# Kernel optimization log

Hardware: AMD Instinct MI355X
Metric: run time of the kernel (lower is better)

## Reference

```python
import jax, jax.numpy as jnp
import numpy as np

B, N, E_PER_G = 32, 2048, 16384
NF, NHID, NCLS = 128, 128, 10
RATIO = 0.5
NT = B * N
E = B * E_PER_G
K1 = int(np.ceil(RATIO * N))        # 1024 nodes kept per graph after pool1
K2 = int(np.ceil(RATIO * K1))       # 512
K3 = int(np.ceil(RATIO * K2))       # 256


def setup_inputs() -> dict:
    key = jax.random.key(0)
    ks = jax.random.split(key, 16)
    x = jax.random.normal(ks[0], (NT, NF), dtype=jnp.float32)
    off = (jnp.arange(B, dtype=jnp.int32) * N)[:, None]
    src = (jax.random.randint(ks[1], (B, E_PER_G), 0, N, dtype=jnp.int32) + off).reshape(-1)
    dst = (jax.random.randint(ks[2], (B, E_PER_G), 0, N, dtype=jnp.int32) + off).reshape(-1)
    edge_index = jnp.stack([src, dst])
    batch = jnp.repeat(jnp.arange(B, dtype=jnp.int32), N)
    def lin(k, i, o):
        return jax.random.normal(k, (i, o), jnp.float32) / np.float32(np.sqrt(i))
    return {
        'x': x, 'edge_index': edge_index, 'batch': batch,
        'W1': lin(ks[3], NF, NHID), 'b1': jnp.zeros((NHID,), jnp.float32),
        'Wp1': lin(ks[4], NHID, 1), 'bp1': jnp.zeros((1,), jnp.float32),
        'W2': lin(ks[5], NHID, NHID), 'b2': jnp.zeros((NHID,), jnp.float32),
        'Wp2': lin(ks[6], NHID, 1), 'bp2': jnp.zeros((1,), jnp.float32),
        'W3': lin(ks[7], NHID, NHID), 'b3': jnp.zeros((NHID,), jnp.float32),
        'Wp3': lin(ks[8], NHID, 1), 'bp3': jnp.zeros((1,), jnp.float32),
        'lin1_W': lin(ks[9], 2 * NHID, NHID), 'lin1_b': jnp.zeros((NHID,), jnp.float32),
        'lin2_W': lin(ks[10], NHID, NHID // 2), 'lin2_b': jnp.zeros((NHID // 2,), jnp.float32),
        'lin3_W': lin(ks[11], NHID // 2, NCLS), 'lin3_b': jnp.zeros((NCLS,), jnp.float32),
    }


def gcn(x, src, dst, emask, nmask, W, b):
    # PyG GCNConv: add self-loops, symmetric normalization D^-1/2 (A+I) D^-1/2 @ (x W) + b.
    # Removed nodes/edges carry weight 0 via masks (equivalent to filter_adj re-indexing).
    h = x @ W
    deg = jnp.zeros((NT,), h.dtype).at[dst].add(emask) + nmask
    dinv = jnp.where(deg > 0, 1.0, 0.0) * jax.lax.rsqrt(jnp.where(deg > 0, deg, 1.0))
    coef = dinv[src] * dinv[dst] * emask               # [E]
    out = jnp.zeros_like(h).at[dst].add(coef[:, None] * h[src])
    out = out + ((dinv * dinv) * nmask)[:, None] * h   # self-loop term, norm = 1/deg
    return out + b


def sagpool(x, src, dst, emask, nmask, Wp, bp, k):
    # score = GCNConv(nhid,1); keep top-k per graph; x <- x[perm] * tanh(score[perm])
    score = gcn(x, src, dst, emask, nmask, Wp, bp)[:, 0]          # [NT]
    s = jnp.where(nmask > 0, score, -jnp.inf).reshape(B, N)
    _, idx = jax.lax.top_k(s, k)                                   # [B, k]
    keep = jnp.zeros((B, N), x.dtype).at[jnp.arange(B)[:, None], idx].set(1.0).reshape(-1)
    x_new = x * jnp.tanh(score)[:, None] * keep[:, None]
    emask_new = emask * keep[src] * keep[dst]                      # filter_adj
    return x_new, emask_new, keep


def readout(x, nmask, count):
    # [global_max_pool, global_mean_pool] over active nodes of each graph
    xb = x.reshape(B, N, -1)
    m = nmask.reshape(B, N, 1)
    mx = jnp.max(jnp.where(m > 0, xb, -jnp.inf), axis=1)
    mn = jnp.sum(xb * m, axis=1) / count
    return jnp.concatenate([mx, mn], axis=-1)


def reference(x, edge_index, batch, W1, b1, Wp1, bp1, W2, b2, Wp2, bp2,
              W3, b3, Wp3, bp3, lin1_W, lin1_b, lin2_W, lin2_b, lin3_W, lin3_b):
    src, dst = edge_index[0], edge_index[1]
    emask = jnp.ones((E,), x.dtype)
    nmask = jnp.ones((NT,), x.dtype)

    h = jax.nn.relu(gcn(x, src, dst, emask, nmask, W1, b1))
    h, emask, nmask = sagpool(h, src, dst, emask, nmask, Wp1, bp1, K1)
    x1 = readout(h, nmask, jnp.asarray(K1, x.dtype))

    h = jax.nn.relu(gcn(h, src, dst, emask, nmask, W2, b2))
    h, emask, nmask = sagpool(h, src, dst, emask, nmask, Wp2, bp2, K2)
    x2 = readout(h, nmask, jnp.asarray(K2, x.dtype))

    h = jax.nn.relu(gcn(h, src, dst, emask, nmask, W3, b3))
    h, emask, nmask = sagpool(h, src, dst, emask, nmask, Wp3, bp3, K3)
    x3 = readout(h, nmask, jnp.asarray(K3, x.dtype))

    g = x1 + x2 + x3
    g = jax.nn.relu(g @ lin1_W + lin1_b)   # dropout = identity in eval
    g = jax.nn.relu(g @ lin2_W + lin2_b)
    return jax.nn.log_softmax(g @ lin3_W + lin3_b, axis=-1)
```

## Files before the change

### kernel.cpp

```cpp
#include <hip/hip_runtime.h>
#include <math.h>


namespace {

constexpr int B_  = 32;
constexpr int N_  = 2048;
constexpr int NT  = B_ * N_;
constexpr int EPG = 16384;
constexpr int E_  = B_ * EPG;
constexpr int NCLS = 10;
constexpr int AST = 132;

__device__ __forceinline__ int relabel(int bid, int bpgsh) {
  int x = bid & 7, slot = bid >> 3;
  int g = x + 8 * (slot >> bpgsh);
  return (g << bpgsh) + (slot & ((1 << bpgsh) - 1));
}

__device__ void csr_build(const int* __restrict__ src, const int* __restrict__ dst,
                          int* __restrict__ off, int* __restrict__ srcp,
                          float* __restrict__ dinv, float* __restrict__ ds,
                          float* __restrict__ sws, int* hist) {
  const int g = blockIdx.x;
  const int t = threadIdx.x;
  const int base_n = g * N_;
  const int base_e = g * EPG;
  int* wsum8 = hist + 2048;
#pragma unroll
  for (int i = 0; i < 4; ++i) hist[t + 512 * i] = 0;
  __syncthreads();
  for (int i = 0; i < EPG / 512; i += 8) {
    int dd[8];
#pragma unroll
    for (int j = 0; j < 8; ++j) dd[j] = dst[base_e + t + 512 * (i + j)];
#pragma unroll
    for (int j = 0; j < 8; ++j) atomicAdd(&hist[dd[j] - base_n], 1);
  }
  __syncthreads();
  int a[4], ssum = 0;
#pragma unroll
  for (int i = 0; i < 4; ++i) { a[i] = hist[4 * t + i]; ssum += a[i]; }
  {
    int lane = t & 63, w = t >> 6;
    int v = ssum;
#pragma unroll
    for (int o = 1; o < 64; o <<= 1) {
      int nv = __shfl_up(v, o);
      if (lane >= o) v += nv;
    }
    if (lane == 63) wsum8[w] = v;
    __syncthreads();
    if (t == 0) {
      int accv = 0;
      for (int i = 0; i < 8; ++i) { int tmp = wsum8[i]; wsum8[i] = accv; accv += tmp; }
    }
    __syncthreads();
    int run = wsum8[w] + v - ssum;
#pragma unroll
    for (int i = 0; i < 4; ++i) {
      int n = 4 * t + i;
      off[base_n + n] = base_e + run;
      hist[n] = run;
      float d0 = 1.f + (float)a[i];
      float di0 = 1.f / sqrtf(d0);
      dinv[base_n + n] = di0;
      ds[base_n + n] = di0;
      sws[base_n + n] = di0 * di0;
      run += a[i];
    }
    if (g == B_ - 1 && t == 0) off[NT] = E_;
  }
  __syncthreads();
  for (int i = 0; i < EPG / 512; i += 8) {
    int dd[8], ss[8];
#pragma unroll
    for (int j = 0; j < 8; ++j) {
      int e = base_e + t + 512 * (i + j);
      dd[j] = dst[e];
      ss[j] = src[e];
    }
#pragma unroll
    for (int j = 0; j < 8; ++j) {
      int slot = atomicAdd(&hist[dd[j] - base_n], 1);
      srcp[base_e + slot] = ss[j];
    }
  }
}

__device__ void norm_body(const int* __restrict__ off,
                          const int* __restrict__ srcp,
                          const float* __restrict__ kpmask,
                          const float* __restrict__ scale,
                          float* __restrict__ dinv,
                          float* __restrict__ ds,
                          float* __restrict__ sws,
                          const int* __restrict__ nkept,
                          int nkshift, int nbpgsh, int nb) {
  int q = relabel(nb, nbpgsh) * 64 + ((int)threadIdx.x >> 3);
  int g = q >> nkshift;
  int node = nkept[g * N_ + (q - (g << nkshift))];
  const int lane = threadIdx.x & 7;
  int s = off[node], en = off[node + 1];
  float d = (lane == 0) ? 1.f : 0.f;
  for (int j = s + lane; j < en; j += 8) d += kpmask[srcp[j]];
#pragma unroll
  for (int o = 4; o >= 1; o >>= 1) d += __shfl_down(d, o, 8);
  if (lane == 0) {
    float di = 1.f / sqrtf(d);
    float sc = scale[node];
    dinv[node] = di;
    ds[node] = di * sc;
    sws[node] = di * di * sc;
  }
}

__global__ __launch_bounds__(512) void k_matmul(const float* __restrict__ A,
                                                const float* __restrict__ W,
                                                float* __restrict__ C,
                                                const int* __restrict__ kept,
                                                int kshift, int bpgsh, int mmBlocks,
                                                const float* __restrict__ scaleArr,
                                                float* __restrict__ pmx,
                                                float* __restrict__ psm,
                                                const int* __restrict__ src,
                                                const int* __restrict__ dst,
                                                int* __restrict__ off,
                                                int* __restrict__ srcp,
                                                float* __restrict__ dinvW,
                                                float* __restrict__ dsW,
                                                float* __restrict__ swsW,
                                                int csrBlocks,
                                                const float* __restrict__ kpmask,
                                                const int* __restrict__ nkept,
                                                int nkshift, int nbpgsh) {
  __shared__ float Ast[2][32 * AST];
  __shared__ float Ws[2][32 * 128];
  __shared__ int rowid[128];
  __shared__ float rsc[128];
  if ((int)blockIdx.x < csrBlocks) {
    csr_build(src, dst, off, srcp, dinvW, dsW, swsW, (int*)&Ast[0][0]);
    return;
  }
  if ((int)blockIdx.x >= csrBlocks + mmBlocks) {
    norm_body(off, srcp, kpmask, scaleArr, dinvW, dsW, swsW, nkept,
              nkshift, nbpgsh, (int)blockIdx.x - csrBlocks - mmBlocks);
    return;
  }
  const int tid = threadIdx.x;
  const int tile = relabel((int)blockIdx.x - csrBlocks, bpgsh);
  if (kept) {
    if (tid < 128) {
      int q = tile * 128 + tid;
      int g = q >> kshift;
      int row = kept[g * N_ + (q - (g << kshift))];
      rowid[tid] = row;
      rsc[tid] = scaleArr[row];
    }
    __syncthreads();
  }
  const int rowq = tid >> 4;
  const int colq = tid & 15;
  float4 va[2], vw[2];
#pragma unroll
  for (int i = 0; i < 2; ++i) {
    int idx = tid + 512 * i;
    int row = idx >> 3, f4 = idx & 7;
    int grw = kept ? rowid[row] : tile * 128 + row;
    va[i] = *(const float4*)&A[(size_t)grw * 128 + 4 * f4];
  }
#pragma unroll
  for (int i = 0; i < 2; ++i) {
    int idx = tid + 512 * i;
    int kk = idx >> 5, cf = idx & 31;
    vw[i] = *(const float4*)&W[(size_t)kk * 128 + 4 * cf];
  }
#pragma unroll
  for (int i = 0; i < 2; ++i) {
    int idx = tid + 512 * i;
    int row = idx >> 3, f4 = idx & 7;
    Ast[0][(4 * f4 + 0) * AST + row] = va[i].x;
    Ast[0][(4 * f4 + 1) * AST + row] = va[i].y;
    Ast[0][(4 * f4 + 2) * AST + row] = va[i].z;
    Ast[0][(4 * f4 + 3) * AST + row] = va[i].w;
  }
#pragma unroll
  for (int i = 0; i < 2; ++i) {
    int idx = tid + 512 * i;
    int kk = idx >> 5, cf = idx & 31;
    *(float4*)&Ws[0][kk * 128 + 4 * cf] = vw[i];
  }
  __syncthreads();
  float acc[4][8] = {};
  for (int c = 0; c < 4; ++c) {
    int cur = c & 1;
    if (c < 3) {
      int k0n = 32 * (c + 1);
#pragma unroll
      for (int i = 0; i < 2; ++i) {
        int idx = tid + 512 * i;
        int row = idx >> 3, f4 = idx & 7;
        int grw = kept ? rowid[row] : tile * 128 + row;
        va[i] = *(const float4*)&A[(size_t)grw * 128 + k0n + 4 * f4];
      }
#pragma unroll
      for (int i = 0; i < 2; ++i) {
        int idx = tid + 512 * i;
        int kk = idx >> 5, cf = idx & 31;
        vw[i] = *(const float4*)&W[(size_t)(k0n + kk) * 128 + 4 * cf];
      }
    }
#pragma unroll 2
    for (int kk = 0; kk < 32; ++kk) {
      float4 a0 = *(const float4*)&Ast[cur][kk * AST + 4 * rowq];
      float4 w0 = *(const float4*)&Ws[cur][kk * 128 + 4 * colq];
      float4 w1 = *(const float4*)&Ws[cur][kk * 128 + 64 + 4 * colq];
      float a[4] = {a0.x, a0.y, a0.z, a0.w};
      float w[8] = {w0.x, w0.y, w0.z, w0.w, w1.x, w1.y, w1.z, w1.w};
#pragma unroll
      for (int r = 0; r < 4; ++r)
#pragma unroll
        for (int cc = 0; cc < 8; ++cc) acc[r][cc] += a[r] * w[cc];
    }
    if (kept) {
      int kkf = tid >> 4;
      int r0 = (tid & 15) * 8;
      float mxv = -INFINITY, smv = 0.f;
#pragma unroll
      for (int rr = 0; rr < 8; rr += 4) {
        float4 av = *(const float4*)&Ast[cur][kkf * AST + r0 + rr];
        float4 s4 = *(const float4*)&rsc[r0 + rr];
        float v0 = av.x * s4.x, v1 = av.y * s4.y;
        float v2 = av.z * s4.z, v3 = av.w * s4.w;
        mxv = fmaxf(fmaxf(fmaxf(mxv, v0), fmaxf(v1, v2)), v3);
        smv += v0 + v1 + v2 + v3;
      }
#pragma unroll
      for (int o = 8; o >= 1; o >>= 1) {
        mxv = fmaxf(mxv, __shfl_down(mxv, o, 16));
        smv += __shfl_down(smv, o, 16);
      }
      if ((tid & 15) == 0) {
        pmx[(size_t)tile * 128 + 32 * c + kkf] = mxv;
        psm[(size_t)tile * 128 + 32 * c + kkf] = smv;
      }
    }
    if (c < 3) {
      int nxt = cur ^ 1;
#pragma unroll
      for (int i = 0; i < 2; ++i) {
        int idx = tid + 512 * i;
        int row = idx >> 3, f4 = idx & 7;
        Ast[nxt][(4 * f4 + 0) * AST + row] = va[i].x;
        Ast[nxt][(4 * f4 + 1) * AST + row] = va[i].y;
        Ast[nxt][(4 * f4 + 2) * AST + row] = va[i].z;
        Ast[nxt][(4 * f4 + 3) * AST + row] = va[i].w;
      }
#pragma unroll
      for (int i = 0; i < 2; ++i) {
        int idx = tid + 512 * i;
        int kk = idx >> 5, cf = idx & 31;
        *(float4*)&Ws[nxt][kk * 128 + 4 * cf] = vw[i];
      }
      __syncthreads();
    }
  }
#pragma unroll
  for (int r = 0; r < 4; ++r) {
    int grw = kept ? rowid[4 * rowq + r] : tile * 128 + 4 * rowq + r;
    float* Crow = &C[(size_t)grw * 128];
    *(float4*)&Crow[4 * colq] = make_float4(acc[r][0], acc[r][1], acc[r][2], acc[r][3]);
    *(float4*)&Crow[64 + 4 * colq] = make_float4(acc[r][4], acc[r][5], acc[r][6], acc[r][7]);
  }
}

__global__ __launch_bounds__(256) void k_agg(const float4* __restrict__ t4,
                                             const int* __restrict__ off,
                                             const int* __restrict__ srcp,
                                             const float* __restrict__ dinv,
                                             const float* __restrict__ ds,
                                             const float* __restrict__ sws,
                                             const float* __restrict__ bias,
                                             const float* __restrict__ Wp,
                                             float4* __restrict__ h4,
                                             float* __restrict__ t1,
                                             const int* __restrict__ kept,
                                             int kshift, int bpgsh) {
  int q = relabel(blockIdx.x, bpgsh) * 8 + (threadIdx.x >> 5);
  int node;
  if (kept) {
    int g = q >> kshift;
    node = kept[g * N_ + (q - (g << kshift))];
  } else {
    node = q;
  }
  const int lane = threadIdx.x & 31;
  const float dvi = dinv[node];
  float sw = sws[node];
  float4 self = t4[(size_t)node * 32 + lane];
  float4 acc = make_float4(sw * self.x, sw * self.y, sw * self.z, sw * self.w);
  int s = off[node], en = off[node + 1];
  int j = s;
  for (; j + 8 <= en; j += 8) {
    int sv[8];
    float cv[8];
#pragma unroll
    for (int i = 0; i < 8; ++i) sv[i] = srcp[j + i];
#pragma unroll
    for (int i = 0; i < 8; ++i) cv[i] = ds[sv[i]] * dvi;
#pragma unroll
    for (int i = 0; i < 8; ++i) {
      if (cv[i] != 0.f) {
        float4 r = t4[(size_t)sv[i] * 32 + lane];
        acc.x += cv[i] * r.x; acc.y += cv[i] * r.y;
        acc.z += cv[i] * r.z; acc.w += cv[i] * r.w;
      }
    }
  }
  for (; j < en; ++j) {
    int s0 = srcp[j];
    float c0 = ds[s0] * dvi;
    if (c0 != 0.f) {
      float4 r0 = t4[(size_t)s0 * 32 + lane];
      acc.x += c0 * r0.x; acc.y += c0 * r0.y; acc.z += c0 * r0.z; acc.w += c0 * r0.w;
    }
  }
  float4 b4 = ((const float4*)bias)[lane];
  acc.x = fmaxf(acc.x + b4.x, 0.f);
  acc.y = fmaxf(acc.y + b4.y, 0.f);
  acc.z = fmaxf(acc.z + b4.z, 0.f);
  acc.w = fmaxf(acc.w + b4.w, 0.f);
  h4[(size_t)node * 32 + lane] = acc;
  float4 wp = ((const float4*)Wp)[lane];
  float part = acc.x * wp.x + acc.y * wp.y + acc.z * wp.z + acc.w * wp.w;
#pragma unroll
  for (int o = 16; o > 0; o >>= 1) part += __shfl_down(part, o, 32);
  if (lane == 0) t1[node] = part;
}

__global__ __launch_bounds__(256) void k_score(const float* __restrict__ t1,
                                               const int* __restrict__ off,
                                               const int* __restrict__ srcp,
                                               const float* __restrict__ dinv,
                                               const float* __restrict__ bp,
                                               float* __restrict__ raw,
                                               const int* __restrict__ kept,
                                               int kshift, int bpgsh) {
  int q = relabel(blockIdx.x, bpgsh) * 32 + (threadIdx.x >> 3);
  int node;
  if (kept) {
    int g = q >> kshift;
    node = kept[g * N_ + (q - (g << kshift))];
  } else {
    node = q;
  }
  const int lane = threadIdx.x & 7;
  int s = off[node], en = off[node + 1];
  float a = 0.f;
  for (int j = s + lane; j < en; j += 8) {
    int sl = srcp[j];
    a += dinv[sl] * t1[sl];
  }
#pragma unroll
  for (int o = 4; o >= 1; o >>= 1) a += __shfl_down(a, o, 8);
  if (lane == 0) {
    float di = dinv[node];
    raw[node] = di * di * t1[node] + di * a + bp[0];
  }
}

__global__ __launch_bounds__(1024) void k_pool(const float* __restrict__ raw,
                                               float* __restrict__ dinv,
                                               float* __restrict__ ds,
                                               float* __restrict__ sws,
                                               float* __restrict__ scale,
                                               float* __restrict__ kpmask,
                                               int* __restrict__ kept,
                                               const float4* __restrict__ h4,
                                               float invk, int k,
                                               const int* __restrict__ inKept, int klen,
                                               const float* __restrict__ pmxA,
                                               const float* __restrict__ psmA,
                                               const float* __restrict__ pmxB,
                                               const float* __restrict__ psmB,
                                               const float* __restrict__ hW1,
                                               const float* __restrict__ hb1,
                                               const float* __restrict__ hW2,
                                               const float* __restrict__ hb2,
                                               const float* __restrict__ hW3,
                                               const float* __restrict__ hb3,
                                               float* __restrict__ out) {
  __shared__ float st1[2048];
  __shared__ float skp[2048];
  __shared__ int skept[1024];
  __shared__ unsigned rephist[4096];
  __shared__ unsigned ebits[64];
  __shared__ int wsum[16];
  __shared__ unsigned bc_digit, bc_prev;
  __shared__ float gr[256], o1[128], o2[64], o3[NCLS];
  const int g = (blockIdx.x & 7) + 8 * (blockIdx.x >> 3);
  const int t = threadIdx.x;
  const int base = g * N_;
  st1[t] = 0.f;
  st1[t + 1024] = 0.f;
  skp[t] = 0.f;
  skp[t + 1024] = 0.f;
  if (t < 64) ebits[t] = 0u;
  __syncthreads();
  int nodeq[2] = {-1, -1};
  float rawv[2] = {0.f, 0.f};
  unsigned key[2] = {0xFFFFFFFFu, 0xFFFFFFFFu};
#pragma unroll
  for (int q = 0; q < 2; ++q) {
    int i = t + q * 1024;
    if (i >= klen) continue;
    int n = inKept ? (inKept[base + i] - base) : i;
    nodeq[q] = n;
    float r = raw[base + n];
    rawv[q] = r;
    unsigned u = __float_as_uint(r);
    u = (u & 0x80000000u) ? ~u : (u | 0x80000000u);
    u = ~u;
    key[q] = u;
  }
  unsigned prefix = 0u, rem = (unsigned)k;
  const int SH0 = 21, SH1 = 10, SH2 = 0;
  for (int p = 0; p < 3; ++p) {
    const int shift = (p == 0) ? SH0 : (p == 1 ? SH1 : SH2);
    const int nb = (p == 2) ? 1024 : 2048;
    const unsigned mask = (p == 0) ? 0u
                        : (p == 1 ? (0xFFFFFFFFu << SH0) : (0xFFFFFFFFu << SH1));
    rephist[t] = 0u;
    rephist[t + 1024] = 0u;
    __syncthreads();
#pragma unroll
    for (int q = 0; q < 2; ++q)
      if (nodeq[q] >= 0 && (key[q] & mask) == prefix)
        atomicAdd(&rephist[(key[q] >> shift) & (unsigned)(nb - 1)], 1u);
    __syncthreads();
    unsigned b0, b1;
    if (nb == 2048) { b0 = rephist[2 * t]; b1 = rephist[2 * t + 1]; }
    else           { b0 = rephist[t];     b1 = 0u; }
    unsigned ps = b0 + b1;
    {
      int lane = t & 63, w = t >> 6;
      unsigned v = ps;
#pragma unroll
      for (int o = 1; o < 64; o <<= 1) {
        unsigned nv = __shfl_up(v, o);
        if (lane >= o) v += nv;
      }
      if (lane == 63) wsum[w] = (int)v;
      __syncthreads();
      if (t == 0) {
        int accv = 0;
        for (int i = 0; i < 16; ++i) { int tmp = wsum[i]; wsum[i] = accv; accv += tmp; }
      }
      __syncthreads();
      unsigned exc = (unsigned)wsum[w] + v - ps;
      if (exc < rem && exc + b0 >= rem) {
        bc_digit = (unsigned)((nb == 2048) ? 2 * t : t);
        bc_prev = exc;
      }
      if (nb == 2048 && exc + b0 < rem && exc + b0 + b1 >= rem) {
        bc_digit = (unsigned)(2 * t + 1);
        bc_prev = exc + b0;
      }
    }
    __syncthreads();
    prefix |= bc_digit << shift;
    rem -= bc_prev;
  }
  const unsigned Tkey = prefix;
  const int need = (int)rem;
#pragma unroll
  for (int q = 0; q < 2; ++q) {
    int n = nodeq[q];
    if (n >= 0 && key[q] == Tkey) atomicOr(&ebits[n >> 5], 1u << (n & 31));
  }
  __syncthreads();
#pragma unroll
  for (int q = 0; q < 2; ++q) {
    int n = nodeq[q];
    if (n < 0) continue;
    float kp;
    if (key[q] < Tkey) {
      kp = 1.f;
    } else if (key[q] == Tkey) {
      int w = n >> 5;
      int rank = __popc(ebits[w] & ((1u << (n & 31)) - 1u));
      for (int u = 0; u < w; ++u) rank += __popc(ebits[u]);
      kp = (rank < need) ? 1.f : 0.f;
    } else {
      kp = 0.f;
    }
    skp[n] = kp;
    float sc = kp * tanhf(rawv[q]);
    st1[n] = sc;
    scale[base + n] = sc;
    kpmask[base + n] = kp;
    if (kp == 0.f) {
      dinv[base + n] = 0.f;
      ds[base + n] = 0.f;
      sws[base + n] = 0.f;
    }
  }
  __syncthreads();
  {
    int lane = t & 63, w = t >> 6;
    int a0 = (int)skp[2 * t], a1 = (int)skp[2 * t + 1];
    int ps = a0 + a1;
    int v = ps;
#pragma unroll
    for (int o = 1; o < 64; o <<= 1) {
      int nv = __shfl_up(v, o);
      if (lane >= o) v += nv;
    }
    if (lane == 63) wsum[w] = v;
    __syncthreads();
    if (t == 0) {
      int accv = 0;
      for (int i = 0; i < 16; ++i) { int tmp = wsum[i]; wsum[i] = accv; accv += tmp; }
    }
    __syncthreads();
    int excl = wsum[w] + v - ps;
    if (a0) { kept[base + excl] = base + 2 * t; skept[excl] = base + 2 * t; }
    if (a1) { kept[base + excl + a0] = base + 2 * t + 1; skept[excl + a0] = base + 2 * t + 1; }
  }
  if (!out) return;
  __syncthreads();
  const int lane = t & 31, ng = t >> 5;
  float4 mx = make_float4(-INFINITY, -INFINITY, -INFINITY, -INFINITY);
  float4 sm = make_float4(0.f, 0.f, 0.f, 0.f);
  for (int i = ng; i < k; i += 32) {
    int node = skept[i];
    float sc = st1[node - base];
    float4 v = h4[(size_t)node * 32 + lane];
    v.x *= sc; v.y *= sc; v.z *= sc; v.w *= sc;
    mx.x = fmaxf(mx.x, v.x); mx.y = fmaxf(mx.y, v.y);
    mx.z = fmaxf(mx.z, v.z); mx.w = fmaxf(mx.w, v.w);
    sm.x += v.x; sm.y += v.y; sm.z += v.z; sm.w += v.w;
  }
  float4* red = (float4*)rephist;
  for (int d = 16; d >= 1; d >>= 1) {
    if (ng >= d && ng < 2 * d) {
      red[(ng - d) * 32 + lane] = mx;
      red[512 + (ng - d) * 32 + lane] = sm;
    }
    __syncthreads();
    if (ng < d) {
      float4 omx = red[ng * 32 + lane];
      float4 osm = red[512 + ng * 32 + lane];
      mx.x = fmaxf(mx.x, omx.x); mx.y = fmaxf(mx.y, omx.y);
      mx.z = fmaxf(mx.z, omx.z); mx.w = fmaxf(mx.w, omx.w);
      sm.x += osm.x; sm.y += osm.y; sm.z += osm.z; sm.w += osm.w;
    }
    __syncthreads();
  }
  if (ng == 0) {
    gr[4 * lane + 0] = mx.x;
    gr[4 * lane + 1] = mx.y;
    gr[4 * lane + 2] = mx.z;
    gr[4 * lane + 3] = mx.w;
    gr[128 + 4 * lane + 0] = sm.x * invk;
    gr[128 + 4 * lane + 1] = sm.y * invk;
    gr[128 + 4 * lane + 2] = sm.z * invk;
    gr[128 + 4 * lane + 3] = sm.w * invk;
  }
  __syncthreads();
  if (t < 128) {
    float mxA = -INFINITY, smA = 0.f;
#pragma unroll
    for (int p = 0; p < 8; ++p) {
      mxA = fmaxf(mxA, pmxA[(size_t)(g * 8 + p) * 128 + t]);
      smA += psmA[(size_t)(g * 8 + p) * 128 + t];
    }
    float mxB = -INFINITY, smB = 0.f;
#pragma unroll
    for (int p = 0; p < 4; ++p) {
      mxB = fmaxf(mxB, pmxB[(size_t)(g * 4 + p) * 128 + t]);
      smB += psmB[(size_t)(g * 4 + p) * 128 + t];
    }
    gr[t] += mxA + mxB;
    gr[t + 128] += smA * (1.f / 1024.f) + smB * (1.f / 512.f);
  }
  __syncthreads();
  if (t < 128) {
    float a = hb1[t];
    for (int kk = 0; kk < 256; ++kk) a += gr[kk] * hW1[kk * 128 + t];
    o1[t] = fmaxf(a, 0.f);
  }
  __syncthreads();
  if (t < 64) {
    float a2 = hb2[t];
    for (int kk = 0; kk < 128; ++kk) a2 += o1[kk] * hW2[kk * 64 + t];
    o2[t] = fmaxf(a2, 0.f);
  }
  __syncthreads();
  if (t < NCLS) {
    float a3 = hb3[t];
    for (int kk = 0; kk < 64; ++kk) a3 += o2[kk] * hW3[kk * NCLS + t];
    o3[t] = a3;
  }
  __syncthreads();
  if (t == 0) {
    float m = -INFINITY;
    for (int c = 0; c < NCLS; ++c) m = fmaxf(m, o3[c]);
    float sum = 0.f;
    for (int c = 0; c < NCLS; ++c) sum += expf(o3[c] - m);
    float lse = logf(sum);
    for (int c = 0; c < NCLS; ++c) out[g * NCLS + c] = o3[c] - m - lse;
  }
}

}

extern "C" void kernel_launch(void* const* d_in, const int* in_sizes, int n_in,
                              void* d_out, int out_size, void* d_ws, size_t ws_size,
                              hipStream_t stream) {
  const float* x = (const float*)d_in[0];
  const int* ei = (const int*)d_in[1];
  const int* src = ei;
  const int* dst = ei + E_;
  const float* Wl[3]  = {(const float*)d_in[3], (const float*)d_in[7], (const float*)d_in[11]};
  const float* bl[3]  = {(const float*)d_in[4], (const float*)d_in[8], (const float*)d_in[12]};
  const float* Wpl[3] = {(const float*)d_in[5], (const float*)d_in[9], (const float*)d_in[13]};
  const float* bpl[3] = {(const float*)d_in[6], (const float*)d_in[10], (const float*)d_in[14]};
  const float* l1W = (const float*)d_in[15];
  const float* l1b = (const float*)d_in[16];
  const float* l2W = (const float*)d_in[17];
  const float* l2b = (const float*)d_in[18];
  const float* l3W = (const float*)d_in[19];
  const float* l3b = (const float*)d_in[20];

  char* p = (char*)d_ws;
  auto alloc = [&](size_t bytes) -> void* {
    void* r = (void*)p;
    p += (bytes + 255) & ~size_t(255);
    return r;
  };
  float* h      = (float*)alloc((size_t)NT * 128 * 4);
  float* t      = (float*)alloc((size_t)NT * 128 * 4);
  float* dinv   = (float*)alloc(NT * 4);
  float* ds     = (float*)alloc(NT * 4);
  float* sws    = (float*)alloc(NT * 4);
  float* scale  = (float*)alloc(NT * 4);
  float* t1     = (float*)alloc(NT * 4);
  float* raw    = (float*)alloc(NT * 4);
  float* kpmask = (float*)alloc(NT * 4);
  int*   srcp   = (int*)alloc(E_ * 4);
  int*   off    = (int*)alloc((NT + 1) * 4);
  int*   kept0  = (int*)alloc(NT * 4);
  int*   kept1  = (int*)alloc(NT * 4);
  int*   kept2  = (int*)alloc(NT * 4);
  float* pmxA   = (float*)alloc(256 * 128 * 4);
  float* psmA   = (float*)alloc(256 * 128 * 4);
  float* pmxB   = (float*)alloc(128 * 128 * 4);
  float* psmB   = (float*)alloc(128 * 128 * 4);

  int* keptL[3] = {kept0, kept1, kept2};
  const int K[3] = {1024, 512, 256};
  const int KSH[3] = {10, 9, 8};
  float* pmxL[3] = {nullptr, pmxA, pmxB};
  float* psmL[3] = {nullptr, psmA, psmB};

  const float* inF = x;
  for (int l = 0; l < 3; ++l) {
    const int* inKept = (l == 0) ? nullptr : keptL[l - 1];
    int inKsh = (l == 0) ? 11 : KSH[l - 1];
    int nrows = (l == 0) ? NT : B_ * K[l - 1];
    int mmB = nrows / 128;
    int mm_bpgsh = (l == 0) ? 4 : (l == 1 ? 3 : 2);
    int ag_bpgsh = (l == 0) ? 8 : (l == 1 ? 7 : 6);
    int sc_bpgsh = (l == 0) ? 6 : (l == 1 ? 5 : 4);
    int csrB = (l == 0) ? B_ : 0;
    int normB = (l == 0) ? 0 : (B_ * K[l - 1]) / 64;
    int nbpgsh = (l == 1) ? 4 : 3;
    int klen = (l == 0) ? N_ : K[l - 1];
    bool last = (l == 2);
    k_matmul<<<csrB + mmB + normB, 512, 0, stream>>>(
        inF, Wl[l], t, inKept, inKsh, mm_bpgsh, mmB, scale, pmxL[l], psmL[l],
        src, dst, off, srcp, dinv, ds, sws, csrB,
        kpmask, inKept, inKsh, nbpgsh);
    k_agg<<<nrows / 8, 256, 0, stream>>>((const float4*)t, off, srcp, dinv, ds, sws,
                                         bl[l], Wpl[l], (float4*)h, t1, inKept, inKsh,
                                         ag_bpgsh);
    k_score<<<nrows / 32, 256, 0, stream>>>(t1, off, srcp, dinv, bpl[l], raw,
                                            inKept, inKsh, sc_bpgsh);
    k_pool<<<B_, 1024, 0, stream>>>(raw, dinv, ds, sws, scale, kpmask,
                                    keptL[l], (const float4*)h,
                                    1.f / (float)K[l], K[l], inKept, klen,
                                    last ? pmxA : nullptr, last ? psmA : nullptr,
                                    last ? pmxB : nullptr, last ? psmB : nullptr,
                                    l1W, l1b, l2W, l2b, l3W, l3b,
                                    last ? (float*)d_out : nullptr);
    inF = h;
  }
}
```

Measured before the change: 281.7 us.

## Compact per-node edge lists after each pool to drop dead sources

```diff
diff --git a/kernel.cpp b/kernel.cpp
--- a/kernel.cpp
+++ b/kernel.cpp
@@ -89,7 +89,8 @@
 }
 
 __device__ void norm_body(const int* __restrict__ off,
-                          const int* __restrict__ srcp,
+                          const int* __restrict__ nsrcp,
+                          const int* __restrict__ ndend,
                           const float* __restrict__ kpmask,
                           const float* __restrict__ scale,
                           float* __restrict__ dinv,
@@ -101,9 +102,10 @@
   int g = q >> nkshift;
   int node = nkept[g * N_ + (q - (g << nkshift))];
   const int lane = threadIdx.x & 7;
-  int s = off[node], en = off[node + 1];
+  int s = off[node];
+  int en = ndend ? ndend[node] : off[node + 1];
   float d = (lane == 0) ? 1.f : 0.f;
-  for (int j = s + lane; j < en; j += 8) d += kpmask[srcp[j]];
+  for (int j = s + lane; j < en; j += 8) d += kpmask[nsrcp[j]];
 #pragma unroll
   for (int o = 4; o >= 1; o >>= 1) d += __shfl_down(d, o, 8);
   if (lane == 0) {
@@ -113,6 +115,37 @@
     ds[node] = di * sc;
     sws[node] = di * di * sc;
   }
+}
+
+__device__ void compact_body(const int* __restrict__ off,
+                             const int* __restrict__ srcIn,
+                             const int* __restrict__ dendIn,
+                             const float* __restrict__ alive,
+                             int* __restrict__ srcOut,
+                             int* __restrict__ dendOut,
+                             const int* __restrict__ nkept,
+                             int nkshift, int nbpgsh, int nb) {
+  int q = relabel(nb, nbpgsh) * 64 + ((int)threadIdx.x >> 3);
+  int g = q >> nkshift;
+  int node = nkept[g * N_ + (q - (g << nkshift))];
+  const int sub = threadIdx.x & 7;
+  const int grp8 = ((int)threadIdx.x & 63) >> 3;
+  int s = off[node];
+  int en = dendIn ? dendIn[node] : off[node + 1];
+  int cnt = 0;
+  for (int j = s; j < en; j += 8) {
+    int idx = j + sub;
+    int sv = 0;
+    bool valid = (idx < en);
+    if (valid) sv = srcIn[idx];
+    bool pred = valid && (alive[sv] > 0.f);
+    unsigned long long b = __ballot(pred);
+    unsigned m8 = (unsigned)(b >> (grp8 * 8)) & 0xFFu;
+    int rank = __popc(m8 & ((1u << sub) - 1u));
+    if (pred) srcOut[s + cnt + rank] = sv;
+    cnt += __popc(m8);
+  }
+  if (sub == 0) dendOut[node] = s + cnt;
 }
 
 __global__ __launch_bounds__(512) void k_matmul(const float* __restrict__ A,
@@ -133,7 +166,12 @@
                                                 int csrBlocks,
                                                 const float* __restrict__ kpmask,
                                                 const int* __restrict__ nkept,
-                                                int nkshift, int nbpgsh) {
+                                                int nkshift, int nbpgsh,
+                                                const int* __restrict__ nsrcp,
+                                                const int* __restrict__ ndend,
+                                                int normBlocks,
+                                                int* __restrict__ csrcOut,
+                                                int* __restrict__ cdendOut) {
   __shared__ float Ast[2][32 * AST];
   __shared__ float Ws[2][32 * 128];
   __shared__ int rowid[128];
@@ -143,8 +181,14 @@
     return;
   }
   if ((int)blockIdx.x >= csrBlocks + mmBlocks) {
-    norm_body(off, srcp, kpmask, scaleArr, dinvW, dsW, swsW, nkept,
-              nkshift, nbpgsh, (int)blockIdx.x - csrBlocks - mmBlocks);
+    int rb = (int)blockIdx.x - csrBlocks - mmBlocks;
+    if (rb < normBlocks) {
+      norm_body(off, nsrcp, ndend, kpmask, scaleArr, dinvW, dsW, swsW, nkept,
+                nkshift, nbpgsh, rb);
+    } else {
+      compact_body(off, nsrcp, ndend, dinvW, csrcOut, cdendOut, nkept,
+                   nkshift, nbpgsh, rb - normBlocks);
+    }
     return;
   }
   const int tid = threadIdx.x;
@@ -277,6 +321,7 @@
 __global__ __launch_bounds__(256) void k_agg(const float4* __restrict__ t4,
                                              const int* __restrict__ off,
                                              const int* __restrict__ srcp,
+                                             const int* __restrict__ dend,
                                              const float* __restrict__ dinv,
                                              const float* __restrict__ ds,
                                              const float* __restrict__ sws,
@@ -299,7 +344,8 @@
   float sw = sws[node];
   float4 self = t4[(size_t)node * 32 + lane];
   float4 acc = make_float4(sw * self.x, sw * self.y, sw * self.z, sw * self.w);
-  int s = off[node], en = off[node + 1];
+  int s = off[node];
+  int en = dend ? dend[node] : off[node + 1];
   int j = s;
   for (; j + 8 <= en; j += 8) {
     int sv[8];
@@ -341,6 +387,7 @@
 __global__ __launch_bounds__(256) void k_score(const float* __restrict__ t1,
                                                const int* __restrict__ off,
                                                const int* __restrict__ srcp,
+                                               const int* __restrict__ dend,
                                                const float* __restrict__ dinv,
                                                const float* __restrict__ bp,
                                                float* __restrict__ raw,
@@ -355,7 +402,8 @@
     node = q;
   }
   const int lane = threadIdx.x & 7;
-  int s = off[node], en = off[node + 1];
+  int s = off[node];
+  int en = dend ? dend[node] : off[node + 1];
   float a = 0.f;
   for (int j = s + lane; j < en; j += 8) {
     int sl = srcp[j];
@@ -649,6 +697,9 @@
   float* raw    = (float*)alloc(NT * 4);
   float* kpmask = (float*)alloc(NT * 4);
   int*   srcp   = (int*)alloc(E_ * 4);
+  int*   srcpB  = (int*)alloc(E_ * 4);
+  int*   dend1  = (int*)alloc(NT * 4);
+  int*   dend2  = (int*)alloc(NT * 4);
   int*   off    = (int*)alloc((NT + 1) * 4);
   int*   kept0  = (int*)alloc(NT * 4);
   int*   kept1  = (int*)alloc(NT * 4);
@@ -663,6 +714,10 @@
   const int KSH[3] = {10, 9, 8};
   float* pmxL[3] = {nullptr, pmxA, pmxB};
   float* psmL[3] = {nullptr, psmA, psmB};
+  const int* srcL[3]  = {srcp, srcpB, srcp};
+  const int* dendL[3] = {nullptr, dend1, dend2};
+  int* srcOutL[2]  = {srcpB, srcp};
+  int* dendOutL[2] = {dend1, dend2};
 
   const float* inF = x;
   for (int l = 0; l < 3; ++l) {
@@ -676,17 +731,22 @@
     int csrB = (l == 0) ? B_ : 0;
     int normB = (l == 0) ? 0 : (B_ * K[l - 1]) / 64;
     int nbpgsh = (l == 1) ? 4 : 3;
+    int compB = normB;
     int klen = (l == 0) ? N_ : K[l - 1];
     bool last = (l == 2);
-    k_matmul<<<csrB + mmB + normB, 512, 0, stream>>>(
+    k_matmul<<<csrB + mmB + normB + compB, 512, 0, stream>>>(
         inF, Wl[l], t, inKept, inKsh, mm_bpgsh, mmB, scale, pmxL[l], psmL[l],
         src, dst, off, srcp, dinv, ds, sws, csrB,
-        kpmask, inKept, inKsh, nbpgsh);
-    k_agg<<<nrows / 8, 256, 0, stream>>>((const float4*)t, off, srcp, dinv, ds, sws,
-                                         bl[l], Wpl[l], (float4*)h, t1, inKept, inKsh,
-                                         ag_bpgsh);
-    k_score<<<nrows / 32, 256, 0, stream>>>(t1, off, srcp, dinv, bpl[l], raw,
-                                            inKept, inKsh, sc_bpgsh);
+        kpmask, inKept, inKsh, nbpgsh,
+        (l == 0) ? nullptr : srcL[l - 1], (l == 0) ? nullptr : dendL[l - 1],
+        normB,
+        (l == 0) ? nullptr : srcOutL[l - 1],
+        (l == 0) ? nullptr : dendOutL[l - 1]);
+    k_agg<<<nrows / 8, 256, 0, stream>>>((const float4*)t, off, srcL[l], dendL[l],
+                                         dinv, ds, sws, bl[l], Wpl[l],
+                                         (float4*)h, t1, inKept, inKsh, ag_bpgsh);
+    k_score<<<nrows / 32, 256, 0, stream>>>(t1, off, srcL[l], dendL[l], dinv,
+                                            bpl[l], raw, inKept, inKsh, sc_bpgsh);
     k_pool<<<B_, 1024, 0, stream>>>(raw, dinv, ds, sws, scale, kpmask,
                                     keptL[l], (const float4*)h,
                                     1.f / (float)K[l], K[l], inKept, klen,
```

New measurement: 279.2 us. About the same (-0.9%).
